# Kernel tuning notes

Hardware: AMD Instinct MI355X
Metric: run time of the kernel (lower is better)

The kernel has to match this reference:

```python
import jax, jax.numpy as jnp
import numpy as np

EMBED = 1024
HEADS = 16
HEAD_DIM = EMBED // HEADS


def setup_inputs() -> dict:
    key = jax.random.key(0)
    ks = jax.random.split(key, 12)
    B, S, D = 4, 2048, EMBED
    scale = 1.0 / np.sqrt(D)
    inp = {
        "query": jax.random.normal(ks[0], (B, S, D), dtype=jnp.float32),
        "key": jax.random.normal(ks[1], (B, S, D), dtype=jnp.float32),
        "value": jax.random.normal(ks[2], (B, S, D), dtype=jnp.float32),
        "Wq": jax.random.normal(ks[3], (D, D), dtype=jnp.float32) * scale,
        "bq": jnp.zeros((D,), dtype=jnp.float32),
        "Wk": jax.random.normal(ks[4], (D, D), dtype=jnp.float32) * scale,
        "bk": jnp.zeros((D,), dtype=jnp.float32),
        "Wv": jax.random.normal(ks[5], (D, D), dtype=jnp.float32) * scale,
        "bv": jnp.zeros((D,), dtype=jnp.float32),
        "Wo": jax.random.normal(ks[6], (D, D), dtype=jnp.float32) * scale,
        "bo": jnp.zeros((D,), dtype=jnp.float32),
    }
    return inp


def reference(query, key, value, Wq, bq, Wk, bk, Wv, bv, Wo, bo):
    B, S, D = query.shape
    H, Dh = HEADS, HEAD_DIM

    def proj(x, W, b):
        # nn.Linear: x @ W.T + b, then split heads -> [B, H, S, Dh]
        y = jnp.einsum('bsd,ed->bse', x, W) + b
        return y.reshape(B, -1, H, Dh).transpose(0, 2, 1, 3)

    q = proj(query, Wq, bq)
    k = proj(key, Wk, bk)
    v = proj(value, Wv, bv)

    attn = jnp.einsum('bhqd,bhkd->bhqk', q, k) / jnp.sqrt(jnp.float32(Dh))
    attn = jax.nn.softmax(attn, axis=-1)
    # dropout: eval mode -> identity
    out = jnp.einsum('bhqk,bhkd->bhqd', attn, v)
    out = out.transpose(0, 2, 1, 3).reshape(B, -1, D)
    out = jnp.einsum('bsd,ed->bse', out, Wo) + bo
    return out
```

## Files before the change

kernel.cpp:

```cpp
#include <hip/hip_runtime.h>
#include <hip/hip_bf16.h>

typedef unsigned short u16;
typedef unsigned int u32;
typedef float f32x4 __attribute__((ext_vector_type(4)));
typedef float f32x16 __attribute__((ext_vector_type(16)));
typedef __bf16 bf16x8 __attribute__((ext_vector_type(8)));
typedef u32 u32x2 __attribute__((ext_vector_type(2)));

#define DEV static __device__ __forceinline__

DEV u16 f2b(float f) { __bf16 h = (__bf16)f; u16 r; __builtin_memcpy(&r, &h, 2); return r; }
DEV u32 pk2(float a, float b) { return (u32)f2b(a) | ((u32)f2b(b) << 16); }
DEV bf16x8 as_bf(uint4 v) { bf16x8 r; __builtin_memcpy(&r, &v, 16); return r; }

#define GLDS(g, l) __builtin_amdgcn_global_load_lds( \
    (__attribute__((address_space(1))) void*)(g),     \
    (__attribute__((address_space(3))) void*)(l), 16, 0, 0)

__global__ __launch_bounds__(256) void conva_k(const float* __restrict__ src,
                                               u16* __restrict__ dst, int n8)
{
  int i = blockIdx.x * 256 + threadIdx.x;
  const int stride = gridDim.x * 256;
  for (; i < n8; i += stride) {
    const float4* p = (const float4*)(src + (size_t)i * 8);
    const float4 a = p[0], b = p[1];
    *(uint4*)(dst + (size_t)i * 8) =
        make_uint4(pk2(a.x, a.y), pk2(a.z, a.w), pk2(b.x, b.y), pk2(b.z, b.w));
  }
}

__global__ __launch_bounds__(256) void convw_k(const float* __restrict__ w0,
                                               const float* __restrict__ w1,
                                               const float* __restrict__ w2,
                                               const float* __restrict__ w3,
                                               u16* __restrict__ dst)
{
  const int seg = blockIdx.x >> 9, sb = blockIdx.x & 511;
  const float* s = seg == 0 ? w0 : seg == 1 ? w1 : seg == 2 ? w2 : w3;
  const int i = sb * 256 + threadIdx.x;
  const float4* p = (const float4*)(s + (size_t)i * 8);
  const float4 a = p[0], b = p[1];
  *(uint4*)(dst + (size_t)seg * 1048576 + (size_t)i * 8) =
      make_uint4(pk2(a.x, a.y), pk2(a.z, a.w), pk2(b.x, b.y), pk2(b.z, b.w));
}

template<int CMODE>
__global__ __launch_bounds__(256) void gemm_b(const u16* __restrict__ A,
                                              const u16* __restrict__ W,
                                              const float* __restrict__ bias,
                                              void* __restrict__ Cp, float scale)
{
  __shared__ u16 lds[2][8192];
  const int tid = threadIdx.x;
  const int lane = tid & 63, w = tid >> 6;
  const int m0 = blockIdx.x * 128, e0 = blockIdx.y * 128;
  const int wr4 = (w >> 1) * 4, wc4 = (w & 1) * 4;

  f32x4 acc[4][4];
#pragma unroll
  for (int i = 0; i < 4; i++)
#pragma unroll
    for (int j = 0; j < 4; j++)
#pragma unroll
      for (int r = 0; r < 4; r++) acc[i][j][r] = 0.f;

  const u16* gA = A + (size_t)(m0 + w * 32 + (lane & 15)) * 1024 + (lane >> 4) * 8;
  const u16* gB = W + (size_t)(e0 + w * 32 + (lane & 15)) * 1024 + (lane >> 4) * 8;

  GLDS(gA,         &lds[0][w * 1024]);
  GLDS(gA + 16384, &lds[0][w * 1024 + 512]);
  GLDS(gB,         &lds[0][4096 + w * 1024]);
  GLDS(gB + 16384, &lds[0][4096 + w * 1024 + 512]);
  __syncthreads();

  int buf = 0;
  const int fo = (lane >> 4) * 128 + (lane & 15) * 8;
  for (int kb = 0; kb < 32; ++kb) {
    const int nbuf = buf ^ 1;
    if (kb < 31) {
      const int k0 = (kb + 1) * 32;
      GLDS(gA + k0,         &lds[nbuf][w * 1024]);
      GLDS(gA + 16384 + k0, &lds[nbuf][w * 1024 + 512]);
      GLDS(gB + k0,         &lds[nbuf][4096 + w * 1024]);
      GLDS(gB + 16384 + k0, &lds[nbuf][4096 + w * 1024 + 512]);
    }
    const u16* la = &lds[buf][0];
    const u16* lb = &lds[buf][4096];
    bf16x8 af[4], bfr[4];
#pragma unroll
    for (int i = 0; i < 4; i++) {
      af[i]  = as_bf(*(const uint4*)(la + (wr4 + i) * 512 + fo));
      bfr[i] = as_bf(*(const uint4*)(lb + (wc4 + i) * 512 + fo));
    }
#pragma unroll
    for (int i = 0; i < 4; i++)
#pragma unroll
      for (int j = 0; j < 4; j++)
        acc[i][j] = __builtin_amdgcn_mfma_f32_16x16x32_bf16(af[i], bfr[j], acc[i][j], 0, 0, 0);
    __syncthreads();
    buf = nbuf;
  }

  const int col = lane & 15, rb4 = (lane >> 4) * 4;
  const int wr = wr4 * 16, wc = wc4 * 16;
#pragma unroll
  for (int j = 0; j < 4; j++) {
    const int e = e0 + wc + j * 16 + col;
    const float bv = bias[e];
#pragma unroll
    for (int i = 0; i < 4; i++) {
#pragma unroll
      for (int r = 0; r < 4; r++) {
        const int m = m0 + wr + i * 16 + rb4 + r;
        const float v = (acc[i][j][r] + bv) * scale;
        if (CMODE == 0) {
          ((float*)Cp)[(size_t)m * 1024 + e] = v;
        } else {
          const int b = m >> 11, s = m & 2047, h = e >> 6, dh = e & 63;
          const size_t bh = (size_t)(b * 16 + h);
          if (CMODE == 2) {
            const size_t idx = (((bh * 64 + (s >> 5)) * 4 + (dh >> 4)) * 64
                                + ((dh >> 3) & 1) * 32 + (s & 31)) * 8 + (dh & 7);
            ((u16*)Cp)[idx] = f2b(v);
          } else {
            const size_t idx = ((bh * 64 + (s >> 5)) * 8 + ((s >> 4) & 1) * 4
                                + (dh >> 5) * 2 + ((s >> 3) & 1)) * 256
                               + (size_t)(dh & 31) * 8 + (s & 7);
            ((u16*)Cp)[idx] = f2b(v);
          }
        }
      }
    }
  }
}

__global__ __launch_bounds__(512, 4) void attn_k(const u16* __restrict__ Qb,
                                                 const u16* __restrict__ Kb,
                                                 const u16* __restrict__ Vb,
                                                 u16* __restrict__ O)
{
  __shared__ u16 kv[2][4096];
  __shared__ u16 ob[8][32][72];
  const int tid = threadIdx.x, wv = tid >> 6, lane = tid & 63;
  const int lo = lane & 31, hi = lane >> 5;
  const int bid = blockIdx.x;
  const int xcd = bid & 7, ix = bid >> 3;
  const int bh = xcd * 8 + (ix & 7);
  const int qb = (ix >> 3) * 8 + wv;
  const int b = bh >> 4, h = bh & 15, q0 = qb * 32;

  const u16* qp = Qb + ((size_t)(bh * 64 + qb) * 4) * 512 + (size_t)lane * 8;
  bf16x8 qf[4];
#pragma unroll
  for (int c = 0; c < 4; c++) qf[c] = as_bf(*(const uint4*)(qp + c * 512));

  const uint4 onesw = make_uint4(0x3F803F80u, 0x3F803F80u, 0x3F803F80u, 0x3F803F80u);
  const bf16x8 ones = as_bf(onesw);

  f32x16 a0, a1, a2;
#pragma unroll
  for (int r = 0; r < 16; r++) { a0[r] = 0.f; a1[r] = 0.f; a2[r] = 0.f; }

  const u16* kp = Kb + (size_t)bh * 131072;
  const u16* vp = Vb + (size_t)bh * 131072;
  const u16* sg = (wv < 4 ? kp + wv * 512 : vp + (wv - 4) * 512) + (size_t)lane * 8;

  GLDS(sg, &kv[0][wv * 512]);
  __syncthreads();

#define ATTN_TILE(CUR, PT, DOPREF)                                            \
  {                                                                           \
    if (DOPREF) GLDS(sg + (size_t)(PT) * 2048, &kv[(CUR) ^ 1][wv * 512]);     \
    const u16* kl = &kv[CUR][0];                                              \
    const u16* vl = &kv[CUR][2048];                                           \
    f32x16 s;                                                                 \
    _Pragma("unroll")                                                         \
    for (int r = 0; r < 16; r++) s[r] = 0.f;                                  \
    __builtin_amdgcn_s_setprio(1);                                            \
    _Pragma("unroll")                                                         \
    for (int c = 0; c < 4; c++)                                               \
      s = __builtin_amdgcn_mfma_f32_32x32x16_bf16(                            \
            as_bf(*(const uint4*)(kl + c * 512 + lane * 8)), qf[c], s, 0, 0, 0); \
    __builtin_amdgcn_s_setprio(0);                                            \
    _Pragma("unroll")                                                         \
    for (int r = 0; r < 16; r++) s[r] = exp2f(s[r]);                          \
    bf16x8 pf[2];                                                             \
    _Pragma("unroll")                                                         \
    for (int kc = 0; kc < 2; kc++) {                                          \
      const u32 A0 = pk2(s[8 * kc + 0], s[8 * kc + 1]);                       \
      const u32 A1 = pk2(s[8 * kc + 2], s[8 * kc + 3]);                       \
      const u32 B0 = pk2(s[8 * kc + 4], s[8 * kc + 5]);                       \
      const u32 B1 = pk2(s[8 * kc + 6], s[8 * kc + 7]);                       \
      u32x2 w02 = __builtin_amdgcn_permlane32_swap(A0, B0, false, false);     \
      u32x2 w13 = __builtin_amdgcn_permlane32_swap(A1, B1, false, false);     \
      pf[kc] = as_bf(make_uint4(w02[0], w13[0], w02[1], w13[1]));             \
    }                                                                         \
    __builtin_amdgcn_s_setprio(1);                                            \
    a0 = __builtin_amdgcn_mfma_f32_32x32x16_bf16(                             \
           as_bf(*(const uint4*)(vl + 0    + lane * 8)), pf[0], a0, 0, 0, 0); \
    a1 = __builtin_amdgcn_mfma_f32_32x32x16_bf16(                             \
           as_bf(*(const uint4*)(vl + 512  + lane * 8)), pf[0], a1, 0, 0, 0); \
    a2 = __builtin_amdgcn_mfma_f32_32x32x16_bf16(ones, pf[0], a2, 0, 0, 0);   \
    a0 = __builtin_amdgcn_mfma_f32_32x32x16_bf16(                             \
           as_bf(*(const uint4*)(vl + 1024 + lane * 8)), pf[1], a0, 0, 0, 0); \
    a1 = __builtin_amdgcn_mfma_f32_32x32x16_bf16(                             \
           as_bf(*(const uint4*)(vl + 1536 + lane * 8)), pf[1], a1, 0, 0, 0); \
    a2 = __builtin_amdgcn_mfma_f32_32x32x16_bf16(ones, pf[1], a2, 0, 0, 0);   \
    __builtin_amdgcn_s_setprio(0);                                            \
    __syncthreads();                                                          \
  }

  for (int t = 0; t < 64; t += 2) {
    ATTN_TILE(0, t + 1, 1)
    ATTN_TILE(1, t + 2, (t + 2 < 64))
  }
#undef ATTN_TILE

  const float inv = 1.f / a2[0];

#pragma unroll
  for (int r = 0; r < 16; r++) {
    const int dh = (r & 3) + 8 * (r >> 2) + 4 * hi;
    ob[wv][lo][dh]      = f2b(a0[r] * inv);
    ob[wv][lo][dh + 32] = f2b(a1[r] * inv);
  }
  const int qr = lane >> 1, hf = lane & 1;
  const u16* src = &ob[wv][qr][hf * 32];
  const uint4 r0 = *(const uint4*)(src + 0);
  const uint4 r1 = *(const uint4*)(src + 8);
  const uint4 r2 = *(const uint4*)(src + 16);
  const uint4 r3 = *(const uint4*)(src + 24);
  const size_t m = (size_t)b * 2048 + q0 + qr;
  uint4* dst = (uint4*)(O + m * 1024 + (size_t)h * 64 + hf * 32);
  dst[0] = r0; dst[1] = r1; dst[2] = r2; dst[3] = r3;
}

extern "C" void kernel_launch(void* const* d_in, const int* in_sizes, int n_in,
                              void* d_out, int out_size, void* d_ws, size_t ws_size,
                              hipStream_t stream)
{
  const float* query = (const float*)d_in[0];
  const float* key   = (const float*)d_in[1];
  const float* value = (const float*)d_in[2];
  const float* Wq = (const float*)d_in[3];
  const float* bq = (const float*)d_in[4];
  const float* Wk = (const float*)d_in[5];
  const float* bk = (const float*)d_in[6];
  const float* Wv = (const float*)d_in[7];
  const float* bv = (const float*)d_in[8];
  const float* Wo = (const float*)d_in[9];
  const float* bo = (const float*)d_in[10];

  const size_t MAT = (size_t)8192 * 1024;
  const size_t WMAT = (size_t)1024 * 1024;
  if (ws_size < (4 * MAT + 4 * WMAT) * sizeof(u16)) return;
  u16* Ac = (u16*)d_ws;
  u16* Wc = Ac + MAT;
  u16* Qw = Wc + 4 * WMAT;
  u16* Kw = Qw + MAT;
  u16* Vw = Kw + MAT;
  u16* Ow = Ac;

  const float qscale = 0.125f * 1.4426950408889634f;

  dim3 bl(256, 1, 1), gg(64, 8);
  hipLaunchKernelGGL(convw_k, dim3(2048), bl, 0, stream, Wq, Wk, Wv, Wo, Wc);

  hipLaunchKernelGGL(conva_k, dim3(2048), bl, 0, stream, query, Ac, (int)(MAT / 8));
  hipLaunchKernelGGL((gemm_b<2>), gg, bl, 0, stream, Ac, Wc + 0 * WMAT, bq, (void*)Qw, qscale);

  hipLaunchKernelGGL(conva_k, dim3(2048), bl, 0, stream, key, Ac, (int)(MAT / 8));
  hipLaunchKernelGGL((gemm_b<2>), gg, bl, 0, stream, Ac, Wc + 1 * WMAT, bk, (void*)Kw, 1.0f);

  hipLaunchKernelGGL(conva_k, dim3(2048), bl, 0, stream, value, Ac, (int)(MAT / 8));
  hipLaunchKernelGGL((gemm_b<3>), gg, bl, 0, stream, Ac, Wc + 2 * WMAT, bv, (void*)Vw, 1.0f);

  hipLaunchKernelGGL(attn_k, dim3(512), dim3(512, 1, 1), 0, stream, Qw, Kw, Vw, Ow);

  hipLaunchKernelGGL((gemm_b<0>), gg, bl, 0, stream, Ow, Wc + 3 * WMAT, bo, d_out, 1.0f);
}
```

Before: 287.4 us.

## Rebalance waves per block in projection GEMM and attention kernels

Measured after the change: 282.0 us. About the same (-1.8%).

```diff
diff --git a/kernel.cpp b/kernel.cpp
--- a/kernel.cpp
+++ b/kernel.cpp
@@ -47,32 +47,30 @@
 }
 
 template<int CMODE>
-__global__ __launch_bounds__(256) void gemm_b(const u16* __restrict__ A,
-                                              const u16* __restrict__ W,
-                                              const float* __restrict__ bias,
-                                              void* __restrict__ Cp, float scale)
+__global__ __launch_bounds__(512, 4) void gemm_b(const u16* __restrict__ A,
+                                                 const u16* __restrict__ W,
+                                                 const float* __restrict__ bias,
+                                                 void* __restrict__ Cp, float scale)
 {
   __shared__ u16 lds[2][8192];
   const int tid = threadIdx.x;
   const int lane = tid & 63, w = tid >> 6;
   const int m0 = blockIdx.x * 128, e0 = blockIdx.y * 128;
-  const int wr4 = (w >> 1) * 4, wc4 = (w & 1) * 4;
-
-  f32x4 acc[4][4];
-#pragma unroll
-  for (int i = 0; i < 4; i++)
+  const int wrb = (w >> 1) * 2, wcb = (w & 1) * 4;
+
+  f32x4 acc[2][4];
+#pragma unroll
+  for (int i = 0; i < 2; i++)
 #pragma unroll
     for (int j = 0; j < 4; j++)
 #pragma unroll
       for (int r = 0; r < 4; r++) acc[i][j][r] = 0.f;
 
-  const u16* gA = A + (size_t)(m0 + w * 32 + (lane & 15)) * 1024 + (lane >> 4) * 8;
-  const u16* gB = W + (size_t)(e0 + w * 32 + (lane & 15)) * 1024 + (lane >> 4) * 8;
-
-  GLDS(gA,         &lds[0][w * 1024]);
-  GLDS(gA + 16384, &lds[0][w * 1024 + 512]);
-  GLDS(gB,         &lds[0][4096 + w * 1024]);
-  GLDS(gB + 16384, &lds[0][4096 + w * 1024 + 512]);
+  const u16* gA = A + (size_t)(m0 + w * 16 + (lane & 15)) * 1024 + (lane >> 4) * 8;
+  const u16* gB = W + (size_t)(e0 + w * 16 + (lane & 15)) * 1024 + (lane >> 4) * 8;
+
+  GLDS(gA, &lds[0][w * 512]);
+  GLDS(gB, &lds[0][4096 + w * 512]);
   __syncthreads();
 
   int buf = 0;
@@ -81,21 +79,20 @@
     const int nbuf = buf ^ 1;
     if (kb < 31) {
       const int k0 = (kb + 1) * 32;
-      GLDS(gA + k0,         &lds[nbuf][w * 1024]);
-      GLDS(gA + 16384 + k0, &lds[nbuf][w * 1024 + 512]);
-      GLDS(gB + k0,         &lds[nbuf][4096 + w * 1024]);
-      GLDS(gB + 16384 + k0, &lds[nbuf][4096 + w * 1024 + 512]);
+      GLDS(gA + k0, &lds[nbuf][w * 512]);
+      GLDS(gB + k0, &lds[nbuf][4096 + w * 512]);
     }
     const u16* la = &lds[buf][0];
     const u16* lb = &lds[buf][4096];
-    bf16x8 af[4], bfr[4];
-#pragma unroll
-    for (int i = 0; i < 4; i++) {
-      af[i]  = as_bf(*(const uint4*)(la + (wr4 + i) * 512 + fo));
-      bfr[i] = as_bf(*(const uint4*)(lb + (wc4 + i) * 512 + fo));
-    }
-#pragma unroll
-    for (int i = 0; i < 4; i++)
+    bf16x8 af[2], bfr[4];
+#pragma unroll
+    for (int i = 0; i < 2; i++)
+      af[i] = as_bf(*(const uint4*)(la + (wrb + i) * 512 + fo));
+#pragma unroll
+    for (int j = 0; j < 4; j++)
+      bfr[j] = as_bf(*(const uint4*)(lb + (wcb + j) * 512 + fo));
+#pragma unroll
+    for (int i = 0; i < 2; i++)
 #pragma unroll
       for (int j = 0; j < 4; j++)
         acc[i][j] = __builtin_amdgcn_mfma_f32_16x16x32_bf16(af[i], bfr[j], acc[i][j], 0, 0, 0);
@@ -104,13 +101,13 @@
   }
 
   const int col = lane & 15, rb4 = (lane >> 4) * 4;
-  const int wr = wr4 * 16, wc = wc4 * 16;
+  const int wr = wrb * 16, wc = wcb * 16;
 #pragma unroll
   for (int j = 0; j < 4; j++) {
     const int e = e0 + wc + j * 16 + col;
     const float bv = bias[e];
 #pragma unroll
-    for (int i = 0; i < 4; i++) {
+    for (int i = 0; i < 2; i++) {
 #pragma unroll
       for (int r = 0; r < 4; r++) {
         const int m = m0 + wr + i * 16 + rb4 + r;
@@ -136,19 +133,19 @@
   }
 }
 
-__global__ __launch_bounds__(512, 4) void attn_k(const u16* __restrict__ Qb,
+__global__ __launch_bounds__(256, 4) void attn_k(const u16* __restrict__ Qb,
                                                  const u16* __restrict__ Kb,
                                                  const u16* __restrict__ Vb,
                                                  u16* __restrict__ O)
 {
   __shared__ u16 kv[2][4096];
-  __shared__ u16 ob[8][32][72];
+  __shared__ u16 ob[4][32][72];
   const int tid = threadIdx.x, wv = tid >> 6, lane = tid & 63;
   const int lo = lane & 31, hi = lane >> 5;
   const int bid = blockIdx.x;
   const int xcd = bid & 7, ix = bid >> 3;
   const int bh = xcd * 8 + (ix & 7);
-  const int qb = (ix >> 3) * 8 + wv;
+  const int qb = (ix >> 3) * 4 + wv;
   const int b = bh >> 4, h = bh & 15, q0 = qb * 32;
 
   const u16* qp = Qb + ((size_t)(bh * 64 + qb) * 4) * 512 + (size_t)lane * 8;
@@ -163,16 +160,19 @@
 #pragma unroll
   for (int r = 0; r < 16; r++) { a0[r] = 0.f; a1[r] = 0.f; a2[r] = 0.f; }
 
-  const u16* kp = Kb + (size_t)bh * 131072;
-  const u16* vp = Vb + (size_t)bh * 131072;
-  const u16* sg = (wv < 4 ? kp + wv * 512 : vp + (wv - 4) * 512) + (size_t)lane * 8;
-
-  GLDS(sg, &kv[0][wv * 512]);
+  const u16* sgK = Kb + (size_t)bh * 131072 + wv * 512 + (size_t)lane * 8;
+  const u16* sgV = Vb + (size_t)bh * 131072 + wv * 512 + (size_t)lane * 8;
+
+  GLDS(sgK, &kv[0][wv * 512]);
+  GLDS(sgV, &kv[0][2048 + wv * 512]);
   __syncthreads();
 
 #define ATTN_TILE(CUR, PT, DOPREF)                                            \
   {                                                                           \
-    if (DOPREF) GLDS(sg + (size_t)(PT) * 2048, &kv[(CUR) ^ 1][wv * 512]);     \
+    if (DOPREF) {                                                             \
+      GLDS(sgK + (size_t)(PT) * 2048, &kv[(CUR) ^ 1][wv * 512]);              \
+      GLDS(sgV + (size_t)(PT) * 2048, &kv[(CUR) ^ 1][2048 + wv * 512]);       \
+    }                                                                         \
     const u16* kl = &kv[CUR][0];                                              \
     const u16* vl = &kv[CUR][2048];                                           \
     f32x16 s;                                                                 \
@@ -265,19 +265,19 @@
 
   const float qscale = 0.125f * 1.4426950408889634f;
 
-  dim3 bl(256, 1, 1), gg(64, 8);
+  dim3 bl(256, 1, 1), bg(512, 1, 1), gg(64, 8);
   hipLaunchKernelGGL(convw_k, dim3(2048), bl, 0, stream, Wq, Wk, Wv, Wo, Wc);
 
   hipLaunchKernelGGL(conva_k, dim3(2048), bl, 0, stream, query, Ac, (int)(MAT / 8));
-  hipLaunchKernelGGL((gemm_b<2>), gg, bl, 0, stream, Ac, Wc + 0 * WMAT, bq, (void*)Qw, qscale);
+  hipLaunchKernelGGL((gemm_b<2>), gg, bg, 0, stream, Ac, Wc + 0 * WMAT, bq, (void*)Qw, qscale);
 
   hipLaunchKernelGGL(conva_k, dim3(2048), bl, 0, stream, key, Ac, (int)(MAT / 8));
-  hipLaunchKernelGGL((gemm_b<2>), gg, bl, 0, stream, Ac, Wc + 1 * WMAT, bk, (void*)Kw, 1.0f);
+  hipLaunchKernelGGL((gemm_b<2>), gg, bg, 0, stream, Ac, Wc + 1 * WMAT, bk, (void*)Kw, 1.0f);
 
   hipLaunchKernelGGL(conva_k, dim3(2048), bl, 0, stream, value, Ac, (int)(MAT / 8));
-  hipLaunchKernelGGL((gemm_b<3>), gg, bl, 0, stream, Ac, Wc + 2 * WMAT, bv, (void*)Vw, 1.0f);
-
-  hipLaunchKernelGGL(attn_k, dim3(512), dim3(512, 1, 1), 0, stream, Qw, Kw, Vw, Ow);
-
-  hipLaunchKernelGGL((gemm_b<0>), gg, bl, 0, stream, Ow, Wc + 3 * WMAT, bo, d_out, 1.0f);
-}
+  hipLaunchKernelGGL((gemm_b<3>), gg, bg, 0, stream, Ac, Wc + 2 * WMAT, bv, (void*)Vw, 1.0f);
+
+  hipLaunchKernelGGL(attn_k, dim3(1024), bl, 0, stream, Qw, Kw, Vw, Ow);
+
+  hipLaunchKernelGGL((gemm_b<0>), gg, bg, 0, stream, Ow, Wc + 3 * WMAT, bo, d_out, 1.0f);
+}
```
